# Kernel tuning notes

Measured on AMD Instinct MI355X. Metric: run time of the kernel, lower is better.

Reference implementation:

```python
import jax, jax.numpy as jnp
import numpy as np

jax.config.update("jax_enable_x64", True)  # I-BERT's FixedPointMul runs in double precision

# I-BERT IntSoftmax constants
COEF0 = 0.35815147
COEF1 = 0.96963238 / COEF0
COEF2 = 1.0 / COEF0
X0 = -0.6931          # -ln(2)
N_EXP = 30            # large integer n in int_exp
MAX_BIT = 32
OUTPUT_BIT = 8
ACT_BIT = 16

B, H, S = 1, 12, 2048


def sg(x):
    return jax.lax.stop_gradient(x)


def ste_round(x):
    # straight-through round (matches torch round_ste / SymmetricQuantFunction backward)
    return x + sg(jnp.round(x) - x)


def ste_floor(x):
    return x + sg(jnp.floor(x) - x)


def sym_scale(x_min, x_max, bits):
    # symmetric_linear_quantization_params: scale = clamp(max(|min|,|max|),1e-8)/(2^(b-1)-1)
    n = 2 ** (bits - 1) - 1
    s = jnp.maximum(jnp.abs(x_min), jnp.abs(x_max))
    return sg(jnp.maximum(s, 1e-8) / n)


def fixedpoint_mul(pre_act, pre_sf, z_sf, bits):
    # I-BERT fixedpoint_mul: requantize pre_act (granularity pre_sf) to scale z_sf
    # using a 31-bit mantissa frexp decomposition, computed in float64.
    n = 2 ** (bits - 1) - 1
    z_int = ste_round(pre_act.astype(jnp.float64) / pre_sf.astype(jnp.float64))
    new_scale = sg((pre_sf / z_sf).astype(jnp.float64))
    e = jnp.floor(jnp.log2(jnp.abs(new_scale))) + 1.0   # frexp exponent
    m_int = jnp.round((new_scale / 2.0 ** e) * 2.0 ** 31)  # 31-bit mantissa
    out = ste_round(z_int * m_int / 2.0 ** (31.0 - e))
    return jnp.clip(out, -n - 1, n).astype(jnp.float32)


def quant_softmax(x):
    n16 = 2 ** (ACT_BIT - 1) - 1
    # ---- outer QuantAct(16, symmetric), specified min/max = data min/max ----
    sf = sym_scale(sg(x.min()), sg(x.max()), ACT_BIT)
    x_int = jnp.clip(ste_round(x / sf), -n16 - 1, n16)
    quant_x = x_int * sf  # dequantized activation returned by QuantAct
    # ---- IntSoftmax ----
    xi = quant_x / sf
    xi = xi - xi.max(axis=-1, keepdims=True)
    # int_exp: shift-based exponential, exp(x) = 2^(-q) * exp(r), r in (-ln2, 0]
    x0_int = sg(jnp.floor(X0 / sf))               # negative integer
    xi = jnp.maximum(xi, N_EXP * x0_int)
    q = ste_floor(xi / x0_int)
    r = xi - x0_int * q
    # int_polynomial: 2nd-order poly approximation of exp on (-ln2, 0]
    b_int = sg(jnp.floor(COEF1 / sf))
    c_int = sg(jnp.floor(COEF2 / sf ** 2))
    z = r * (r + b_int) + c_int
    exp_sf = sg(COEF0 * sf ** 2) / 2.0 ** N_EXP
    exp_int = jnp.maximum(ste_floor(z * 2.0 ** (N_EXP - q)), 0.0)
    # ---- inner QuantAct(16): requantize exp to 16 bits to avoid overflow ----
    act_sf = sym_scale(sg(exp_int.min()), sg(exp_int.max()), ACT_BIT)
    exp_int16 = fixedpoint_mul(exp_int, exp_sf, act_sf, ACT_BIT)
    # ---- integer normalization to output_bit fixed point ----
    s = exp_int16.sum(axis=-1, keepdims=True)
    factor = ste_floor(2.0 ** MAX_BIT / s)
    out_int = ste_floor(exp_int16 * factor / 2.0 ** (MAX_BIT - OUTPUT_BIT))
    out_sf = 1.0 / 2.0 ** OUTPUT_BIT
    return out_int * out_sf  # softmax probs quantized to 1/256 grid


def setup_inputs() -> dict:
    key = jax.random.key(0)
    x = jax.random.normal(key, (B, H, S, S), dtype=jnp.float32)
    return {"x": x}


def reference(x):
    return quant_softmax(x)
```

## Files before the change

kernel.cpp:

```cpp
#include <hip/hip_runtime.h>
#include <math.h>


#define ROW_S 2048
#define MM_BLOCKS 2048

typedef float floatx4 __attribute__((ext_vector_type(4)));

struct Scalars {
    double exp_sf_d;
    double inv_exp_sf;
    double m_int;
    double inv_pow;
    float  sf;
    float  inv_sf;
    float  x0_int;
    float  inv_x0;
    float  b_int;
    float  c_int;
    float  thirty_x0;
    float  _pad;
};

__device__ __forceinline__ float div_rn(float a, float b, float inv) {
    const float q0 = __fmul_rn(a, inv);
    const float r  = __fmaf_rn(-b, q0, a);
    return __fmaf_rn(r, inv, q0);
}
__device__ __forceinline__ double ddiv_rn(double a, double b, double inv) {
    const double q0 = __dmul_rn(a, inv);
    const double r  = __fma_rn(-b, q0, a);
    return __fma_rn(r, inv, q0);
}

__global__ __launch_bounds__(256) void k_minmax(const float* __restrict__ x,
                                                float* __restrict__ pmin,
                                                float* __restrict__ pmax,
                                                int n4) {
    const int tid = threadIdx.x;
    float vmin = INFINITY, vmax = -INFINITY;
    const float4* x4 = (const float4*)x;
    for (int i = blockIdx.x * 256 + tid; i < n4; i += MM_BLOCKS * 256) {
        float4 v = x4[i];
        vmin = fminf(vmin, fminf(fminf(v.x, v.y), fminf(v.z, v.w)));
        vmax = fmaxf(vmax, fmaxf(fmaxf(v.x, v.y), fmaxf(v.z, v.w)));
    }
#pragma unroll
    for (int m = 32; m > 0; m >>= 1) {
        vmin = fminf(vmin, __shfl_xor(vmin, m));
        vmax = fmaxf(vmax, __shfl_xor(vmax, m));
    }
    __shared__ float smin[4], smax[4];
    const int wave = tid >> 6, lane = tid & 63;
    if (lane == 0) { smin[wave] = vmin; smax[wave] = vmax; }
    __syncthreads();
    if (tid == 0) {
        pmin[blockIdx.x] = fminf(fminf(smin[0], smin[1]), fminf(smin[2], smin[3]));
        pmax[blockIdx.x] = fmaxf(fmaxf(smax[0], smax[1]), fmaxf(smax[2], smax[3]));
    }
}

__global__ __launch_bounds__(256) void k_scalars(const float* __restrict__ pmin,
                                                 const float* __restrict__ pmax,
                                                 Scalars* __restrict__ sc) {
    const int tid = threadIdx.x;
    float vmin = INFINITY, vmax = -INFINITY;
    for (int i = tid; i < MM_BLOCKS; i += 256) {
        vmin = fminf(vmin, pmin[i]);
        vmax = fmaxf(vmax, pmax[i]);
    }
#pragma unroll
    for (int m = 32; m > 0; m >>= 1) {
        vmin = fminf(vmin, __shfl_xor(vmin, m));
        vmax = fmaxf(vmax, __shfl_xor(vmax, m));
    }
    __shared__ float smin[4], smax[4];
    const int wave = tid >> 6, lane = tid & 63;
    if (lane == 0) { smin[wave] = vmin; smax[wave] = vmax; }
    __syncthreads();
    if (tid == 0) {
        const float xmin = fminf(fminf(smin[0], smin[1]), fminf(smin[2], smin[3]));
        const float xmax = fmaxf(fmaxf(smax[0], smax[1]), fmaxf(smax[2], smax[3]));
        const float sabs  = fmaxf(fabsf(xmin), fabsf(xmax));
        const float sf    = __fdiv_rn(fmaxf(sabs, 1e-8f), 32767.0f);
        const float x0i   = floorf(__fdiv_rn((float)(-0.6931), sf));
        const float sfsq  = __fmul_rn(sf, sf);
        const float b_int = floorf(__fdiv_rn((float)(0.96963238 / 0.35815147), sf));
        const float c_int = floorf(__fdiv_rn((float)(1.0 / 0.35815147), sfsq));
        const float exp_sf = __fdiv_rn(__fmul_rn((float)(0.35815147), sfsq), 1073741824.0f);
        const float emax   = __fmul_rn(c_int, 1073741824.0f);
        const float act_sf = __fdiv_rn(fmaxf(emax, 1e-8f), 32767.0f);
        const float  nsf = __fdiv_rn(exp_sf, act_sf);
        const double ns  = (double)nsf;
        int E;
        (void)frexp(ns, &E);
        const double m_int = rint(ldexp(ns, 31 - E));
        sc->exp_sf_d   = (double)exp_sf;
        sc->inv_exp_sf = 1.0 / (double)exp_sf;
        sc->m_int      = m_int;
        sc->inv_pow    = ldexp(1.0, E - 31);
        sc->sf         = sf;
        sc->inv_sf     = __fdiv_rn(1.0f, sf);
        sc->x0_int     = x0i;
        sc->inv_x0     = __fdiv_rn(1.0f, x0i);
        sc->b_int      = b_int;
        sc->c_int      = c_int;
        sc->thirty_x0  = __fmul_rn(30.0f, x0i);
    }
}

__global__ __launch_bounds__(256) void k_row(const float* __restrict__ x,
                                             float* __restrict__ out,
                                             const Scalars* __restrict__ scp) {
    const int tid = threadIdx.x;
    const size_t rowbase = (size_t)blockIdx.x * ROW_S;
    const float4* x4 = (const float4*)(x + rowbase);
    floatx4* o4 = (floatx4*)(out + rowbase);

    const float4 va = x4[tid];
    const float4 vb = x4[tid + 256];

    const Scalars sc = *scp;
    const float sf = sc.sf, inv_sf = sc.inv_sf;

    float xv[8] = {va.x, va.y, va.z, va.w, vb.x, vb.y, vb.z, vb.w};

    float xi[8];
    float vmax = -INFINITY;
#pragma unroll
    for (int j = 0; j < 8; ++j) {
        float t = rintf(div_rn(xv[j], sf, inv_sf));
        t = fminf(fmaxf(t, -32768.0f), 32767.0f);
        t = __fmul_rn(t, sf);
        t = div_rn(t, sf, inv_sf);
        xi[j] = t;
        vmax = fmaxf(vmax, t);
    }

    __shared__ float red[8];
    const int wave = tid >> 6, lane = tid & 63;
#pragma unroll
    for (int m = 32; m > 0; m >>= 1) vmax = fmaxf(vmax, __shfl_xor(vmax, m));
    if (lane == 0) red[wave] = vmax;
    __syncthreads();
    const float ximax = fmaxf(fmaxf(red[0], red[1]), fmaxf(red[2], red[3]));

    float e16[8];
    float ssum = 0.0f;
#pragma unroll
    for (int j = 0; j < 8; ++j) {
        const float xs = __fsub_rn(xi[j], ximax);
        const float xm = fmaxf(xs, sc.thirty_x0);
        const float qf = floorf(div_rn(xm, sc.x0_int, sc.inv_x0));
        const float r  = __fsub_rn(xm, __fmul_rn(sc.x0_int, qf));
        const float z  = __fadd_rn(__fmul_rn(r, __fadd_rn(r, sc.b_int)), sc.c_int);
        const int   qi = (int)qf;
        const float p2 = __int_as_float((157 - qi) << 23);
        const float ei = fmaxf(floorf(__fmul_rn(z, p2)), 0.0f);
        const double a  = (double)ei;
        const double zi = rint(ddiv_rn(a, sc.exp_sf_d, sc.inv_exp_sf));
        double ov = rint(__dmul_rn(__dmul_rn(zi, sc.m_int), sc.inv_pow));
        ov = fmin(fmax(ov, -32768.0), 32767.0);
        const float v = (float)ov;
        e16[j] = v;
        ssum += v;
    }

#pragma unroll
    for (int m = 32; m > 0; m >>= 1) ssum += __shfl_xor(ssum, m);
    if (lane == 0) red[4 + wave] = ssum;
    __syncthreads();
    const float s = ((red[4] + red[5]) + (red[6] + red[7]));
    const float factor = floorf(__fdiv_rn(4294967296.0f, s));

    float ov[8];
#pragma unroll
    for (int j = 0; j < 8; ++j) {
        const float oi = floorf(__fmul_rn(__fmul_rn(e16[j], factor), 5.9604644775390625e-8f));
        ov[j] = __fmul_rn(oi, 0.00390625f);
    }
    floatx4 w0 = {ov[0], ov[1], ov[2], ov[3]};
    floatx4 w1 = {ov[4], ov[5], ov[6], ov[7]};
    __builtin_nontemporal_store(w0, &o4[tid]);
    __builtin_nontemporal_store(w1, &o4[tid + 256]);
}

extern "C" void kernel_launch(void* const* d_in, const int* in_sizes, int n_in,
                              void* d_out, int out_size, void* d_ws, size_t ws_size,
                              hipStream_t stream) {
    const float* x = (const float*)d_in[0];
    float* out = (float*)d_out;
    const int n = in_sizes[0];
    const int rows = n / ROW_S;

    Scalars* sc = (Scalars*)d_ws;
    float* pmin = (float*)((char*)d_ws + 256);
    float* pmax = pmin + MM_BLOCKS;

    k_minmax<<<MM_BLOCKS, 256, 0, stream>>>(x, pmin, pmax, n / 4);
    k_scalars<<<1, 256, 0, stream>>>(pmin, pmax, sc);
    k_row<<<rows, 256, 0, stream>>>(x, out, sc);
}
```

Before: 355.1 us.

## Compute per-row raw max in the min/max pass to drop row-kernel max reduction

```diff
diff --git a/kernel.cpp b/kernel.cpp
--- a/kernel.cpp
+++ b/kernel.cpp
@@ -3,7 +3,8 @@
 
 
 #define ROW_S 2048
-#define MM_BLOCKS 2048
+#define RPB 8
+#define P1_BLOCKS (24576 / RPB)
 
 typedef float floatx4 __attribute__((ext_vector_type(4)));
 
@@ -33,55 +34,47 @@
     return __fma_rn(r, inv, q0);
 }
 
-__global__ __launch_bounds__(256) void k_minmax(const float* __restrict__ x,
-                                                float* __restrict__ pmin,
-                                                float* __restrict__ pmax,
-                                                int n4) {
-    const int tid = threadIdx.x;
-    float vmin = INFINITY, vmax = -INFINITY;
+__global__ __launch_bounds__(256) void k_rowmax(const float* __restrict__ x,
+                                                float* __restrict__ pabs,
+                                                float* __restrict__ rowmax) {
+    const int t   = threadIdx.x;
+    const int rib = t >> 5;
+    const int lir = t & 31;
+    const size_t base4 = ((size_t)blockIdx.x * RPB + rib) * (ROW_S / 4) + lir;
     const float4* x4 = (const float4*)x;
-    for (int i = blockIdx.x * 256 + tid; i < n4; i += MM_BLOCKS * 256) {
-        float4 v = x4[i];
-        vmin = fminf(vmin, fminf(fminf(v.x, v.y), fminf(v.z, v.w)));
+
+    float vmax = -INFINITY, amax = 0.0f;
+#pragma unroll
+    for (int k = 0; k < 16; ++k) {
+        float4 v = x4[base4 + (size_t)k * 32];
         vmax = fmaxf(vmax, fmaxf(fmaxf(v.x, v.y), fmaxf(v.z, v.w)));
+        amax = fmaxf(amax, fmaxf(fmaxf(fabsf(v.x), fabsf(v.y)),
+                                 fmaxf(fabsf(v.z), fabsf(v.w))));
     }
 #pragma unroll
-    for (int m = 32; m > 0; m >>= 1) {
-        vmin = fminf(vmin, __shfl_xor(vmin, m));
-        vmax = fmaxf(vmax, __shfl_xor(vmax, m));
-    }
-    __shared__ float smin[4], smax[4];
+    for (int m = 16; m > 0; m >>= 1) vmax = fmaxf(vmax, __shfl_xor(vmax, m));
+    if (lir == 0) rowmax[blockIdx.x * RPB + rib] = vmax;
+#pragma unroll
+    for (int m = 32; m > 0; m >>= 1) amax = fmaxf(amax, __shfl_xor(amax, m));
+    __shared__ float sa[4];
+    if ((t & 63) == 0) sa[t >> 6] = amax;
+    __syncthreads();
+    if (t == 0) pabs[blockIdx.x] = fmaxf(fmaxf(sa[0], sa[1]), fmaxf(sa[2], sa[3]));
+}
+
+__global__ __launch_bounds__(256) void k_scalars(const float* __restrict__ pabs,
+                                                 Scalars* __restrict__ sc) {
+    const int tid = threadIdx.x;
+    float amax = 0.0f;
+    for (int i = tid; i < P1_BLOCKS; i += 256) amax = fmaxf(amax, pabs[i]);
+#pragma unroll
+    for (int m = 32; m > 0; m >>= 1) amax = fmaxf(amax, __shfl_xor(amax, m));
+    __shared__ float sa[4];
     const int wave = tid >> 6, lane = tid & 63;
-    if (lane == 0) { smin[wave] = vmin; smax[wave] = vmax; }
+    if (lane == 0) sa[wave] = amax;
     __syncthreads();
     if (tid == 0) {
-        pmin[blockIdx.x] = fminf(fminf(smin[0], smin[1]), fminf(smin[2], smin[3]));
-        pmax[blockIdx.x] = fmaxf(fmaxf(smax[0], smax[1]), fmaxf(smax[2], smax[3]));
-    }
-}
-
-__global__ __launch_bounds__(256) void k_scalars(const float* __restrict__ pmin,
-                                                 const float* __restrict__ pmax,
-                                                 Scalars* __restrict__ sc) {
-    const int tid = threadIdx.x;
-    float vmin = INFINITY, vmax = -INFINITY;
-    for (int i = tid; i < MM_BLOCKS; i += 256) {
-        vmin = fminf(vmin, pmin[i]);
-        vmax = fmaxf(vmax, pmax[i]);
-    }
-#pragma unroll
-    for (int m = 32; m > 0; m >>= 1) {
-        vmin = fminf(vmin, __shfl_xor(vmin, m));
-        vmax = fmaxf(vmax, __shfl_xor(vmax, m));
-    }
-    __shared__ float smin[4], smax[4];
-    const int wave = tid >> 6, lane = tid & 63;
-    if (lane == 0) { smin[wave] = vmin; smax[wave] = vmax; }
-    __syncthreads();
-    if (tid == 0) {
-        const float xmin = fminf(fminf(smin[0], smin[1]), fminf(smin[2], smin[3]));
-        const float xmax = fmaxf(fmaxf(smax[0], smax[1]), fmaxf(smax[2], smax[3]));
-        const float sabs  = fmaxf(fabsf(xmin), fabsf(xmax));
+        const float sabs = fmaxf(fmaxf(sa[0], sa[1]), fmaxf(sa[2], sa[3]));
         const float sf    = __fdiv_rn(fmaxf(sabs, 1e-8f), 32767.0f);
         const float x0i   = floorf(__fdiv_rn((float)(-0.6931), sf));
         const float sfsq  = __fmul_rn(sf, sf);
@@ -111,7 +104,8 @@
 
 __global__ __launch_bounds__(256) void k_row(const float* __restrict__ x,
                                              float* __restrict__ out,
-                                             const Scalars* __restrict__ scp) {
+                                             const Scalars* __restrict__ scp,
+                                             const float* __restrict__ rowmax) {
     const int tid = threadIdx.x;
     const size_t rowbase = (size_t)blockIdx.x * ROW_S;
     const float4* x4 = (const float4*)(x + rowbase);
@@ -119,37 +113,30 @@
 
     const float4 va = x4[tid];
     const float4 vb = x4[tid + 256];
+    const float  rm = rowmax[blockIdx.x];
 
     const Scalars sc = *scp;
     const float sf = sc.sf, inv_sf = sc.inv_sf;
 
+    float ximax;
+    {
+        float t = rintf(div_rn(rm, sf, inv_sf));
+        t = fminf(fmaxf(t, -32768.0f), 32767.0f);
+        t = __fmul_rn(t, sf);
+        ximax = div_rn(t, sf, inv_sf);
+    }
+
     float xv[8] = {va.x, va.y, va.z, va.w, vb.x, vb.y, vb.z, vb.w};
 
-    float xi[8];
-    float vmax = -INFINITY;
+    float e16[8];
+    float ssum = 0.0f;
 #pragma unroll
     for (int j = 0; j < 8; ++j) {
         float t = rintf(div_rn(xv[j], sf, inv_sf));
         t = fminf(fmaxf(t, -32768.0f), 32767.0f);
         t = __fmul_rn(t, sf);
         t = div_rn(t, sf, inv_sf);
-        xi[j] = t;
-        vmax = fmaxf(vmax, t);
-    }
-
-    __shared__ float red[8];
-    const int wave = tid >> 6, lane = tid & 63;
-#pragma unroll
-    for (int m = 32; m > 0; m >>= 1) vmax = fmaxf(vmax, __shfl_xor(vmax, m));
-    if (lane == 0) red[wave] = vmax;
-    __syncthreads();
-    const float ximax = fmaxf(fmaxf(red[0], red[1]), fmaxf(red[2], red[3]));
-
-    float e16[8];
-    float ssum = 0.0f;
-#pragma unroll
-    for (int j = 0; j < 8; ++j) {
-        const float xs = __fsub_rn(xi[j], ximax);
+        const float xs = __fsub_rn(t, ximax);
         const float xm = fmaxf(xs, sc.thirty_x0);
         const float qf = floorf(div_rn(xm, sc.x0_int, sc.inv_x0));
         const float r  = __fsub_rn(xm, __fmul_rn(sc.x0_int, qf));
@@ -166,11 +153,13 @@
         ssum += v;
     }
 
+    __shared__ float red[4];
+    const int wave = tid >> 6, lane = tid & 63;
 #pragma unroll
     for (int m = 32; m > 0; m >>= 1) ssum += __shfl_xor(ssum, m);
-    if (lane == 0) red[4 + wave] = ssum;
+    if (lane == 0) red[wave] = ssum;
     __syncthreads();
-    const float s = ((red[4] + red[5]) + (red[6] + red[7]));
+    const float s = ((red[0] + red[1]) + (red[2] + red[3]));
     const float factor = floorf(__fdiv_rn(4294967296.0f, s));
 
     float ov[8];
@@ -193,11 +182,11 @@
     const int n = in_sizes[0];
     const int rows = n / ROW_S;
 
-    Scalars* sc = (Scalars*)d_ws;
-    float* pmin = (float*)((char*)d_ws + 256);
-    float* pmax = pmin + MM_BLOCKS;
+    Scalars* sc   = (Scalars*)d_ws;
+    float* pabs   = (float*)((char*)d_ws + 256);
+    float* rowmax = (float*)((char*)d_ws + 32768);
 
-    k_minmax<<<MM_BLOCKS, 256, 0, stream>>>(x, pmin, pmax, n / 4);
-    k_scalars<<<1, 256, 0, stream>>>(pmin, pmax, sc);
-    k_row<<<rows, 256, 0, stream>>>(x, out, sc);
+    k_rowmax<<<P1_BLOCKS, 256, 0, stream>>>(x, pabs, rowmax);
+    k_scalars<<<1, 256, 0, stream>>>(pabs, sc);
+    k_row<<<rows, 256, 0, stream>>>(x, out, sc, rowmax);
 }
```

New measurement: 360.7 us. No clear change (+1.6%).
